# Kernel optimization log

Measured on AMD Instinct MI355X. Metric: run time of the kernel, lower is better.

The kernel has to match this reference:

```python
import jax, jax.numpy as jnp
import numpy as np

EPS = 1e-5
H = W = 14  # spatial grid, N = H*W = 196


def layernorm(x, g, b):
    m = x.mean(-1, keepdims=True)
    v = ((x - m) ** 2).mean(-1, keepdims=True)
    return (x - m) * jax.lax.rsqrt(v + EPS) * g + b


def fem_step(x, s):
    # x: [B, C, H, W]; blockwise instance-norm -> sigmoid gate -> 0.5*x + 0.5*attn*x
    B, C, h, w = x.shape
    nbh = -(-h // s)
    nbw = -(-w // s)
    idh = np.arange(h) // s
    idw = np.arange(w) // s
    bid_np = (idh[:, None] * nbw + idw[None, :]).reshape(-1)  # [h*w]
    cnt = jnp.asarray(np.bincount(bid_np, minlength=nbh * nbw).astype(np.float32))
    bid = jnp.asarray(bid_np)
    xt = x.reshape(B, C, h * w).transpose(2, 0, 1)  # [HW, B, C]
    s1 = jax.ops.segment_sum(xt, bid, num_segments=nbh * nbw)      # [nblk, B, C]
    s2 = jax.ops.segment_sum(xt * xt, bid, num_segments=nbh * nbw)
    mean = s1 / cnt[:, None, None]
    var = s2 / cnt[:, None, None] - mean * mean  # biased var, as F.instance_norm
    attn = jax.nn.sigmoid((xt - mean[bid]) * jax.lax.rsqrt(var[bid] + EPS))
    out = 0.5 * xt * (1.0 + attn)  # 0.5*x + 0.5*attn*x
    return out.transpose(1, 2, 0).reshape(B, C, h, w)


def fem(x):
    # p=[2,1,0] -> block sizes H//4=3, H//2=7, H//1=14
    for s in (H // 4, H // 2, H):
        x = fem_step(x, s)
    return x


def setup_inputs() -> dict:
    key = jax.random.key(0)
    ks = jax.random.split(key, 4)
    B, N, C = 64, H * W, 1024
    hid = 4 * C
    return {
        "x": jax.random.normal(ks[0], (B, N, C), jnp.float32),
        "ln1_g": jnp.ones((C,), jnp.float32),
        "ln1_b": jnp.zeros((C,), jnp.float32),
        "cw": jax.random.normal(ks[1], (H, W // 2 + 1, C, 2), jnp.float32) * 0.02,
        "ln2_g": jnp.ones((C,), jnp.float32),
        "ln2_b": jnp.zeros((C,), jnp.float32),
        "fc1_w": jax.random.normal(ks[2], (C, hid), jnp.float32) * 0.02,
        "fc1_b": jnp.zeros((hid,), jnp.float32),
        "fc2_w": jax.random.normal(ks[3], (hid, C), jnp.float32) * 0.02,
        "fc2_b": jnp.zeros((C,), jnp.float32),
    }


def reference(x, ln1_g, ln1_b, cw, ln2_g, ln2_b, fc1_w, fc1_b, fc2_w, fc2_b):
    B, N, C = x.shape
    # FFT global filter
    y = layernorm(x, ln1_g, ln1_b)
    yf = jnp.fft.rfft2(y.reshape(B, H, W, C), axes=(1, 2), norm="ortho")
    yf = yf * (cw[..., 0] + 1j * cw[..., 1])
    y = jnp.fft.irfft2(yf, s=(H, W), axes=(1, 2), norm="ortho").reshape(B, N, C)
    # MLP
    y = layernorm(y, ln2_g, ln2_b)
    y = jax.nn.gelu(y @ fc1_w + fc1_b, approximate=False) @ fc2_w + fc2_b
    # FEM on [B, C, H, W]
    y = fem(y.transpose(0, 2, 1).reshape(B, C, H, W))
    y = y.reshape(B, C, N).transpose(0, 2, 1)
    return x + y
```

## Files before the change

kernel.cpp:

```cpp
#include <hip/hip_runtime.h>

constexpr int CB = 64;
constexpr int CHH = 14, CWW = 14;
constexpr int CN = 196;
constexpr int CC = 1024;
constexpr int CROWS = CB * CN;
constexpr int CKW = 8;

constexpr float C14[14] = {
  1.0f, 0.9009688679024191f, 0.6234898018587336f, 0.2225209339563144f,
  -0.2225209339563144f, -0.6234898018587336f, -0.9009688679024191f, -1.0f,
  -0.9009688679024191f, -0.6234898018587336f, -0.2225209339563144f,
  0.2225209339563144f, 0.6234898018587336f, 0.9009688679024191f };
constexpr float S14[14] = {
  0.0f, 0.4338837391175581f, 0.7818314824680298f, 0.9749279121818236f,
  0.9749279121818236f, 0.7818314824680298f, 0.4338837391175581f, 0.0f,
  -0.4338837391175581f, -0.7818314824680298f, -0.9749279121818236f,
  -0.9749279121818236f, -0.7818314824680298f, -0.4338837391175581f };

typedef __attribute__((ext_vector_type(8))) short bf16x8;
typedef __attribute__((ext_vector_type(4))) float f32x4;

__device__ __forceinline__ unsigned short f2bf(float f) {
  unsigned u = __builtin_bit_cast(unsigned, f);
  u += 0x7FFFu + ((u >> 16) & 1u);
  return (unsigned short)(u >> 16);
}
__device__ __forceinline__ float bf2f(unsigned short h) {
  return __builtin_bit_cast(float, (unsigned)h << 16);
}

__device__ __forceinline__ void gload_lds16(const void* g, void* l) {
  __builtin_amdgcn_global_load_lds(
      (const __attribute__((address_space(1))) void*)g,
      (__attribute__((address_space(3))) void*)l, 16, 0, 0);
}

#define WAITV(N)  asm volatile("s_waitcnt vmcnt(" #N ")" ::: "memory")
#define SBAR()    asm volatile("s_barrier" ::: "memory")
#define WAITLGKM0() asm volatile("s_waitcnt lgkmcnt(0)" ::: "memory")

template<int OUTBF>
__global__ __launch_bounds__(256)
void ln_kernel(const float* __restrict__ in, const float* __restrict__ gam,
               const float* __restrict__ bet, float* __restrict__ outf,
               unsigned short* __restrict__ outb)
{
  const int row = blockIdx.x;
  const int t = threadIdx.x;
  const float4 v = *(const float4*)(in + (size_t)row * CC + t * 4);
  float s  = v.x + v.y + v.z + v.w;
  float s2 = v.x*v.x + v.y*v.y + v.z*v.z + v.w*v.w;
  #pragma unroll
  for (int o = 32; o > 0; o >>= 1) { s += __shfl_down(s, o); s2 += __shfl_down(s2, o); }
  __shared__ float red[8];
  const int wid = t >> 6, lane = t & 63;
  if (lane == 0) { red[wid] = s; red[4 + wid] = s2; }
  __syncthreads();
  s  = red[0] + red[1] + red[2] + red[3];
  s2 = red[4] + red[5] + red[6] + red[7];
  const float mean = s * (1.0f / CC);
  const float var  = s2 * (1.0f / CC) - mean * mean;
  const float r = rsqrtf(var + 1e-5f);
  const float4 g4 = *(const float4*)(gam + t * 4);
  const float4 b4 = *(const float4*)(bet + t * 4);
  const float o0 = (v.x - mean) * r * g4.x + b4.x;
  const float o1 = (v.y - mean) * r * g4.y + b4.y;
  const float o2 = (v.z - mean) * r * g4.z + b4.z;
  const float o3 = (v.w - mean) * r * g4.w + b4.w;
  if (OUTBF) {
    ushort4 p; p.x = f2bf(o0); p.y = f2bf(o1); p.z = f2bf(o2); p.w = f2bf(o3);
    *(ushort4*)(outb + (size_t)row * CC + t * 4) = p;
  } else {
    *(float4*)(outf + (size_t)row * CC + t * 4) = make_float4(o0, o1, o2, o3);
  }
}

__global__ __launch_bounds__(256)
void fft_w_fwd(const float* __restrict__ y, float* __restrict__ Ar, float* __restrict__ Ai)
{
  const int t = threadIdx.x;
  const int bid = blockIdx.x;
  const int cc = bid & 3;
  const int tmp = bid >> 2;
  const int h = tmp % 14;
  const int b = tmp / 14;
  const int c = cc * 256 + t;
  const size_t base = ((size_t)b * CN + (size_t)h * CWW) * CC + c;
  float v[14];
  #pragma unroll
  for (int w = 0; w < 14; w++) v[w] = y[base + (size_t)w * CC];
  const size_t obase = (((size_t)b * CHH + h) * CKW) * CC + c;
  #pragma unroll
  for (int kw = 0; kw < 8; kw++) {
    float sr = 0.f, si = 0.f;
    #pragma unroll
    for (int w = 0; w < 14; w++) {
      const int m = (w * kw) % 14;
      sr += v[w] * C14[m];
      si -= v[w] * S14[m];
    }
    Ar[obase + (size_t)kw * CC] = sr;
    Ai[obase + (size_t)kw * CC] = si;
  }
}

__global__ __launch_bounds__(256)
void fft_h_filt(const float* __restrict__ Ar, const float* __restrict__ Ai,
                const float* __restrict__ cw, float* __restrict__ Br, float* __restrict__ Bi)
{
  const int t = threadIdx.x;
  const int bid = blockIdx.x;
  const int cc = bid & 3;
  const int tmp = bid >> 2;
  const int kw = tmp & 7;
  const int b = tmp >> 3;
  const int c = cc * 256 + t;
  const size_t base = (((size_t)b * CHH) * CKW + kw) * CC + c;
  float ar[14], ai[14];
  #pragma unroll
  for (int h = 0; h < 14; h++) {
    ar[h] = Ar[base + (size_t)h * (CKW * CC)];
    ai[h] = Ai[base + (size_t)h * (CKW * CC)];
  }
  float fr[14], fi[14];
  #pragma unroll
  for (int kh = 0; kh < 14; kh++) {
    float yr = 0.f, yi = 0.f;
    #pragma unroll
    for (int h = 0; h < 14; h++) {
      const int m = (h * kh) % 14;
      yr += ar[h] * C14[m] + ai[h] * S14[m];
      yi += ai[h] * C14[m] - ar[h] * S14[m];
    }
    const size_t widx = (((size_t)kh * CKW + kw) * CC + c) * 2;
    const float wr = cw[widx], wi = cw[widx + 1];
    fr[kh] = yr * wr - yi * wi;
    fi[kh] = yr * wi + yi * wr;
  }
  #pragma unroll
  for (int h = 0; h < 14; h++) {
    float sr = 0.f, si = 0.f;
    #pragma unroll
    for (int kh = 0; kh < 14; kh++) {
      const int m = (h * kh) % 14;
      sr += fr[kh] * C14[m] - fi[kh] * S14[m];
      si += fr[kh] * S14[m] + fi[kh] * C14[m];
    }
    Br[base + (size_t)h * (CKW * CC)] = sr;
    Bi[base + (size_t)h * (CKW * CC)] = si;
  }
}

__global__ __launch_bounds__(256)
void fft_w_inv(const float* __restrict__ Br, const float* __restrict__ Bi, float* __restrict__ y2)
{
  const int t = threadIdx.x;
  const int bid = blockIdx.x;
  const int cc = bid & 3;
  const int tmp = bid >> 2;
  const int h = tmp % 14;
  const int b = tmp / 14;
  const int c = cc * 256 + t;
  const size_t ibase = (((size_t)b * CHH + h) * CKW) * CC + c;
  float br[8], bi[8];
  #pragma unroll
  for (int k = 0; k < 8; k++) {
    br[k] = Br[ibase + (size_t)k * CC];
    bi[k] = Bi[ibase + (size_t)k * CC];
  }
  const size_t obase = ((size_t)b * CN + (size_t)h * CWW) * CC + c;
  #pragma unroll
  for (int w = 0; w < 14; w++) {
    float s = br[0] + ((w & 1) ? -br[7] : br[7]);
    #pragma unroll
    for (int k = 1; k < 7; k++) {
      const int m = (w * k) % 14;
      s += 2.0f * (br[k] * C14[m] - bi[k] * S14[m]);
    }
    y2[obase + (size_t)w * CC] = s * (1.0f / 196.0f);
  }
}

__global__ __launch_bounds__(256)
void transpose_f32_bf16(const float* __restrict__ in, unsigned short* __restrict__ out,
                        int R, int Ccols)
{
  __shared__ float tile[32][33];
  const int tx = threadIdx.x & 31;
  const int ty = threadIdx.x >> 5;
  const int cb = blockIdx.x * 32;
  const int rb = blockIdx.y * 32;
  #pragma unroll
  for (int i = 0; i < 32; i += 8)
    tile[ty + i][tx] = in[(size_t)(rb + ty + i) * Ccols + cb + tx];
  __syncthreads();
  #pragma unroll
  for (int i = 0; i < 32; i += 8)
    out[(size_t)(cb + ty + i) * R + rb + tx] = f2bf(tile[tx][ty + i]);
}

#define STAGE(REG, TILE_, DST) do {                                           \
  const unsigned short* _g = (((REG) < 2) ? A : BT);                          \
  const int _gb = (((REG) < 2) ? brow : bcol);                                \
  int _r0, _r1;                                                               \
  if ((REG) == 0)      { _r0 = vA;       _r1 = 128 + vA; }                    \
  else if ((REG) == 1) { _r0 = 64 + vA;  _r1 = 192 + vA; }                    \
  else if ((REG) == 2) { _r0 = ((vA>>5)<<6) + (vA&31);      _r1 = _r0 + 128; }\
  else                 { _r0 = ((vA>>5)<<6) + 32 + (vA&31); _r1 = _r0 + 128; }\
  const int _gc = (TILE_) * 64 + cl;                                          \
  gload_lds16(_g + (size_t)(_gb + _r0) * K + _gc, (DST) + _r0 * 128 + dcol16);\
  gload_lds16(_g + (size_t)(_gb + _r1) * K + _gc, (DST) + _r1 * 128 + dcol16);\
} while (0)

#define PHASE(TT, CA, CB, NA, NB, PH) do {                                    \
  if (((PH) & 1) == 0) {                                                      \
    const int mh_ = (PH) >> 1;                                                \
    _Pragma("unroll")                                                         \
    for (int mf = 0; mf < 4; ++mf) {                                          \
      const int row = wm * 128 + mh_ * 64 + mf * 16 + lrow;                   \
      const int sw = (row & 7) << 4;                                          \
      af[mf][0] = *(const bf16x8*)((CA) + row * 128 + ((0  | dq) ^ sw));      \
      af[mf][1] = *(const bf16x8*)((CA) + row * 128 + ((64 | dq) ^ sw));      \
    }                                                                         \
  }                                                                           \
  {                                                                           \
    const int nh_ = (PH) & 1;                                                 \
    _Pragma("unroll")                                                         \
    for (int nf = 0; nf < 2; ++nf) {                                          \
      const int row = wn * 64 + (nh_ * 2 + nf) * 16 + lrow;                   \
      const int sw = (row & 7) << 4;                                          \
      bfr[nf][0] = *(const bf16x8*)((CB) + row * 128 + ((0  | dq) ^ sw));     \
      bfr[nf][1] = *(const bf16x8*)((CB) + row * 128 + ((64 | dq) ^ sw));     \
    }                                                                         \
  }                                                                           \
  if ((TT) + 1 < NT) {                                                        \
    if ((PH) == 0)      STAGE(0, (TT)+1, NA);                                 \
    else if ((PH) == 1) STAGE(2, (TT)+1, NB);                                 \
    else if ((PH) == 2) STAGE(3, (TT)+1, NB);                                 \
    else                STAGE(1, (TT)+1, NA);                                 \
  }                                                                           \
  if ((PH) == 0)      { if ((TT) == NT - 1) { WAITV(0); } else { WAITV(6); } }\
  else if ((PH) == 1) { WAITV(6); }                                           \
  else if ((PH) == 2) { WAITV(6); }                                           \
  SBAR();                                                                     \
  WAITLGKM0();                                                                \
  __builtin_amdgcn_sched_barrier(0);                                          \
  __builtin_amdgcn_s_setprio(1);                                              \
  {                                                                           \
    const int mh_ = (PH) >> 1, nh_ = (PH) & 1;                                \
    _Pragma("unroll")                                                         \
    for (int ks = 0; ks < 2; ++ks)                                            \
      _Pragma("unroll")                                                       \
      for (int mf = 0; mf < 4; ++mf)                                          \
        _Pragma("unroll")                                                     \
        for (int nf = 0; nf < 2; ++nf)                                        \
          acc[mh_ * 4 + mf][nh_ * 2 + nf] = __builtin_amdgcn_mfma_f32_16x16x32_bf16( \
              af[mf][ks], bfr[nf][ks], acc[mh_ * 4 + mf][nh_ * 2 + nf], 0, 0, 0); \
  }                                                                           \
  __builtin_amdgcn_s_setprio(0);                                              \
} while (0)

#define KTILE(TT, CA, CB, NA, NB) do {                                        \
  PHASE(TT, CA, CB, NA, NB, 0); PHASE(TT, CA, CB, NA, NB, 1);                 \
  PHASE(TT, CA, CB, NA, NB, 2); PHASE(TT, CA, CB, NA, NB, 3);                 \
} while (0)

template<int DO_GELU>
__global__ __launch_bounds__(512, 2)
void gemm256(const unsigned short* __restrict__ A, const unsigned short* __restrict__ BT,
             const float* __restrict__ bias, unsigned short* __restrict__ C,
             int M, int N, int K)
{
  __shared__ __align__(16) short A0s[256 * 64];
  __shared__ __align__(16) short A1s[256 * 64];
  __shared__ __align__(16) short B0s[256 * 64];
  __shared__ __align__(16) short B1s[256 * 64];
  char* a0 = (char*)A0s; char* a1 = (char*)A1s;
  char* b0 = (char*)B0s; char* b1 = (char*)B1s;

  const int t = threadIdx.x;
  const int wid = t >> 6, lane = t & 63;
  const int wm = wid >> 2, wn = wid & 3;
  const int lrow = lane & 15, qk = lane >> 4;
  const int dq = qk << 4;

  const int nbx = N >> 8, nby = M >> 8;
  const int nwg = nbx * nby;
  const int orig = blockIdx.x;
  const int q8 = nwg >> 3, r8 = nwg & 7, xcd = orig & 7, lid = orig >> 3;
  const int wg = (xcd < r8 ? xcd * (q8 + 1) : r8 * (q8 + 1) + (xcd - r8) * q8) + lid;
  const int gw = 4 * nby;
  const int gid = wg / gw, rem = wg % gw;
  const int bx = gid * 4 + (rem & 3);
  const int by = rem >> 2;
  const int brow = by << 8, bcol = bx << 8;
  const int NT = K >> 6;

  const int vA = t >> 3;
  const int cl = ((t ^ (t >> 3)) & 7) << 3;
  const int dcol16 = (t & 7) << 4;

  f32x4 acc[8][4] = {};
  bf16x8 af[4][2], bfr[2][2];

  STAGE(0, 0, a0); STAGE(2, 0, b0); STAGE(3, 0, b0); STAGE(1, 0, a0);
  WAITV(0);
  SBAR();

  for (int T = 0; T < NT; T += 2) {
    KTILE(T,     a0, b0, a1, b1);
    KTILE(T + 1, a1, b1, a0, b0);
  }

  #pragma unroll
  for (int mf = 0; mf < 8; ++mf) {
    #pragma unroll
    for (int nf = 0; nf < 4; ++nf) {
      const int ccol = bcol + wn * 64 + nf * 16 + lrow;
      const float bb = bias[ccol];
      #pragma unroll
      for (int j = 0; j < 4; ++j) {
        const int r = brow + wm * 128 + mf * 16 + qk * 4 + j;
        float v = acc[mf][nf][j] + bb;
        if (DO_GELU) v = 0.5f * v * (1.0f + erff(v * 0.70710678118654752f));
        C[(size_t)r * N + ccol] = f2bf(v);
      }
    }
  }
}

__device__ __forceinline__ void fem_block(unsigned short* col, int t,
                                          int h0, int nh, int w0, int nw)
{
  float s = 0.f, s2 = 0.f;
  for (int ih = 0; ih < nh; ih++)
    for (int iw = 0; iw < nw; iw++) {
      const float v = bf2f(col[((h0 + ih) * 14 + w0 + iw) * 128 + t]);
      s += v; s2 += v * v;
    }
  const float inv = 1.0f / (float)(nh * nw);
  const float m = s * inv;
  const float var = s2 * inv - m * m;
  const float r = rsqrtf(var + 1e-5f);
  for (int ih = 0; ih < nh; ih++)
    for (int iw = 0; iw < nw; iw++) {
      const int idx = ((h0 + ih) * 14 + w0 + iw) * 128 + t;
      const float v = bf2f(col[idx]);
      const float a = 1.0f / (1.0f + __expf(-(v - m) * r));
      col[idx] = f2bf(0.5f * v * (1.0f + a));
    }
}

__global__ __launch_bounds__(128)
void fem_kernel(const unsigned short* __restrict__ z, const float* __restrict__ x,
                float* __restrict__ out)
{
  __shared__ unsigned short buf[CN * 128];
  const int t = threadIdx.x;
  const int b = blockIdx.x >> 3;
  const int cc = blockIdx.x & 7;
  const int c = cc * 128 + t;
  const size_t base = (size_t)b * CN * CC + c;
  #pragma unroll 4
  for (int n = 0; n < CN; n++) buf[n * 128 + t] = z[base + (size_t)n * CC];
  const int st3[5] = {0, 3, 6, 9, 12};
  const int ln3[5] = {3, 3, 3, 3, 2};
  for (int i = 0; i < 5; i++)
    for (int j = 0; j < 5; j++)
      fem_block(buf, t, st3[i], ln3[i], st3[j], ln3[j]);
  for (int i = 0; i < 2; i++)
    for (int j = 0; j < 2; j++)
      fem_block(buf, t, i * 7, 7, j * 7, 7);
  fem_block(buf, t, 0, 14, 0, 14);
  #pragma unroll 4
  for (int n = 0; n < CN; n++)
    out[base + (size_t)n * CC] = x[base + (size_t)n * CC] + bf2f(buf[n * 128 + t]);
}

extern "C" void kernel_launch(void* const* d_in, const int* in_sizes, int n_in,
                              void* d_out, int out_size, void* d_ws, size_t ws_size,
                              hipStream_t stream) {
  const float* x     = (const float*)d_in[0];
  const float* ln1_g = (const float*)d_in[1];
  const float* ln1_b = (const float*)d_in[2];
  const float* cw    = (const float*)d_in[3];
  const float* ln2_g = (const float*)d_in[4];
  const float* ln2_b = (const float*)d_in[5];
  const float* fc1_w = (const float*)d_in[6];
  const float* fc1_b = (const float*)d_in[7];
  const float* fc2_w = (const float*)d_in[8];
  const float* fc2_b = (const float*)d_in[9];
  float* out = (float*)d_out;
  char* ws = (char*)d_ws;

  const size_t SZ_A = (size_t)CB * CHH * CKW * CC * 4;
  float* Ar = (float*)(ws);
  float* Ai = (float*)(ws + SZ_A);
  float* Br = (float*)(ws + 2 * SZ_A);
  float* Bi = (float*)(ws + 3 * SZ_A);
  unsigned short* A1   = (unsigned short*)(ws);
  unsigned short* W1T  = (unsigned short*)(ws + SZ_A);
  unsigned short* W2T  = (unsigned short*)(ws + SZ_A + (size_t)4096 * 1024 * 2);
  unsigned short* Hmid = (unsigned short*)(ws + 2 * SZ_A);
  unsigned short* Z    = (unsigned short*)(ws);

  ln_kernel<0><<<CROWS, 256, 0, stream>>>(x, ln1_g, ln1_b, out, nullptr);
  fft_w_fwd<<<CB * CHH * 4, 256, 0, stream>>>(out, Ar, Ai);
  fft_h_filt<<<CB * CKW * 4, 256, 0, stream>>>(Ar, Ai, cw, Br, Bi);
  fft_w_inv<<<CB * CHH * 4, 256, 0, stream>>>(Br, Bi, out);
  ln_kernel<1><<<CROWS, 256, 0, stream>>>(out, ln2_g, ln2_b, nullptr, A1);
  transpose_f32_bf16<<<dim3(4096 / 32, 1024 / 32), 256, 0, stream>>>(fc1_w, W1T, 1024, 4096);
  transpose_f32_bf16<<<dim3(1024 / 32, 4096 / 32), 256, 0, stream>>>(fc2_w, W2T, 4096, 1024);
  gemm256<1><<<dim3(784), 512, 0, stream>>>(A1, W1T, fc1_b, Hmid, CROWS, 4096, 1024);
  gemm256<0><<<dim3(196), 512, 0, stream>>>(Hmid, W2T, fc2_b, Z, CROWS, 1024, 4096);
  fem_kernel<<<CB * 8, 128, 0, stream>>>(Z, x, out);
}
```

Before: 493.4 us.

## Restructure GEMM K-loop to one barrier per tile and reuse B fragments

```diff
diff --git a/kernel.cpp b/kernel.cpp
--- a/kernel.cpp
+++ b/kernel.cpp
@@ -213,57 +213,62 @@
   gload_lds16(_g + (size_t)(_gb + _r1) * K + _gc, (DST) + _r1 * 128 + dcol16);\
 } while (0)
 
-#define PHASE(TT, CA, CB, NA, NB, PH) do {                                    \
-  if (((PH) & 1) == 0) {                                                      \
-    const int mh_ = (PH) >> 1;                                                \
+#define LOADA(CAarr, MH) do {                                                 \
+  _Pragma("unroll")                                                           \
+  for (int mf = 0; mf < 4; ++mf) {                                            \
+    const int row = wm * 128 + (MH) * 64 + mf * 16 + lrow;                    \
+    const int sw = (row & 7) << 4;                                            \
+    af[mf][0] = *(const bf16x8*)((CAarr) + row * 128 + ((0  | dq) ^ sw));     \
+    af[mf][1] = *(const bf16x8*)((CAarr) + row * 128 + ((64 | dq) ^ sw));     \
+  }                                                                           \
+} while (0)
+
+#define LOADB(CBarr, DEST, NH) do {                                           \
+  _Pragma("unroll")                                                           \
+  for (int nf = 0; nf < 2; ++nf) {                                            \
+    const int row = wn * 64 + ((NH) * 2 + nf) * 16 + lrow;                    \
+    const int sw = (row & 7) << 4;                                            \
+    DEST[nf][0] = *(const bf16x8*)((CBarr) + row * 128 + ((0  | dq) ^ sw));   \
+    DEST[nf][1] = *(const bf16x8*)((CBarr) + row * 128 + ((64 | dq) ^ sw));   \
+  }                                                                           \
+} while (0)
+
+#define MFMA8(MH, NH, BFR) do {                                               \
+  _Pragma("unroll")                                                           \
+  for (int ks = 0; ks < 2; ++ks)                                              \
     _Pragma("unroll")                                                         \
-    for (int mf = 0; mf < 4; ++mf) {                                          \
-      const int row = wm * 128 + mh_ * 64 + mf * 16 + lrow;                   \
-      const int sw = (row & 7) << 4;                                          \
-      af[mf][0] = *(const bf16x8*)((CA) + row * 128 + ((0  | dq) ^ sw));      \
-      af[mf][1] = *(const bf16x8*)((CA) + row * 128 + ((64 | dq) ^ sw));      \
-    }                                                                         \
+    for (int mf = 0; mf < 4; ++mf)                                            \
+      _Pragma("unroll")                                                       \
+      for (int nf = 0; nf < 2; ++nf)                                          \
+        acc[(MH) * 4 + mf][(NH) * 2 + nf] = __builtin_amdgcn_mfma_f32_16x16x32_bf16( \
+            af[mf][ks], BFR[nf][ks], acc[(MH) * 4 + mf][(NH) * 2 + nf], 0, 0, 0); \
+} while (0)
+
+#define TILEBODY(TT, CAarr, CBarr, NAarr, NBarr) do {                         \
+  WAITV(0);                                                                   \
+  SBAR();                                                                     \
+  LOADA(CAarr, 0);                                                            \
+  LOADB(CBarr, bf0, 0);                                                       \
+  LOADB(CBarr, bf1, 1);                                                       \
+  if ((TT) + 1 < NT) {                                                        \
+    STAGE(0, (TT)+1, NAarr);                                                  \
+    STAGE(2, (TT)+1, NBarr);                                                  \
+    STAGE(3, (TT)+1, NBarr);                                                  \
+    STAGE(1, (TT)+1, NAarr);                                                  \
   }                                                                           \
-  {                                                                           \
-    const int nh_ = (PH) & 1;                                                 \
-    _Pragma("unroll")                                                         \
-    for (int nf = 0; nf < 2; ++nf) {                                          \
-      const int row = wn * 64 + (nh_ * 2 + nf) * 16 + lrow;                   \
-      const int sw = (row & 7) << 4;                                          \
-      bfr[nf][0] = *(const bf16x8*)((CB) + row * 128 + ((0  | dq) ^ sw));     \
-      bfr[nf][1] = *(const bf16x8*)((CB) + row * 128 + ((64 | dq) ^ sw));     \
-    }                                                                         \
-  }                                                                           \
-  if ((TT) + 1 < NT) {                                                        \
-    if ((PH) == 0)      STAGE(0, (TT)+1, NA);                                 \
-    else if ((PH) == 1) STAGE(2, (TT)+1, NB);                                 \
-    else if ((PH) == 2) STAGE(3, (TT)+1, NB);                                 \
-    else                STAGE(1, (TT)+1, NA);                                 \
-  }                                                                           \
-  if ((PH) == 0)      { if ((TT) == NT - 1) { WAITV(0); } else { WAITV(6); } }\
-  else if ((PH) == 1) { WAITV(6); }                                           \
-  else if ((PH) == 2) { WAITV(6); }                                           \
-  SBAR();                                                                     \
   WAITLGKM0();                                                                \
   __builtin_amdgcn_sched_barrier(0);                                          \
   __builtin_amdgcn_s_setprio(1);                                              \
-  {                                                                           \
-    const int mh_ = (PH) >> 1, nh_ = (PH) & 1;                                \
-    _Pragma("unroll")                                                         \
-    for (int ks = 0; ks < 2; ++ks)                                            \
-      _Pragma("unroll")                                                       \
-      for (int mf = 0; mf < 4; ++mf)                                          \
-        _Pragma("unroll")                                                     \
-        for (int nf = 0; nf < 2; ++nf)                                        \
-          acc[mh_ * 4 + mf][nh_ * 2 + nf] = __builtin_amdgcn_mfma_f32_16x16x32_bf16( \
-              af[mf][ks], bfr[nf][ks], acc[mh_ * 4 + mf][nh_ * 2 + nf], 0, 0, 0); \
-  }                                                                           \
+  MFMA8(0, 0, bf0);                                                           \
+  MFMA8(0, 1, bf1);                                                           \
   __builtin_amdgcn_s_setprio(0);                                              \
-} while (0)
-
-#define KTILE(TT, CA, CB, NA, NB) do {                                        \
-  PHASE(TT, CA, CB, NA, NB, 0); PHASE(TT, CA, CB, NA, NB, 1);                 \
-  PHASE(TT, CA, CB, NA, NB, 2); PHASE(TT, CA, CB, NA, NB, 3);                 \
+  LOADA(CAarr, 1);                                                            \
+  WAITLGKM0();                                                                \
+  __builtin_amdgcn_sched_barrier(0);                                          \
+  __builtin_amdgcn_s_setprio(1);                                              \
+  MFMA8(1, 0, bf0);                                                           \
+  MFMA8(1, 1, bf1);                                                           \
+  __builtin_amdgcn_s_setprio(0);                                              \
 } while (0)
 
 template<int DO_GELU>
@@ -302,15 +307,13 @@
   const int dcol16 = (t & 7) << 4;
 
   f32x4 acc[8][4] = {};
-  bf16x8 af[4][2], bfr[2][2];
+  bf16x8 af[4][2], bf0[2][2], bf1[2][2];
 
   STAGE(0, 0, a0); STAGE(2, 0, b0); STAGE(3, 0, b0); STAGE(1, 0, a0);
-  WAITV(0);
-  SBAR();
 
   for (int T = 0; T < NT; T += 2) {
-    KTILE(T,     a0, b0, a1, b1);
-    KTILE(T + 1, a1, b1, a0, b0);
+    TILEBODY(T,     a0, b0, a1, b1);
+    TILEBODY(T + 1, a1, b1, a0, b0);
   }
 
   #pragma unroll
```

After: 486.8 us. About the same (-1.3%).
